# Kernel optimization log

Hardware: AMD Instinct MI355X
Metric: run time of the kernel (lower is better)

## Reference

```python
import jax, jax.numpy as jnp
import numpy as np

QMIN_A, QMAX_A = -128.0, 127.0  # int8 activation range
QMIN_W, QMAX_W = -8, 7          # int4 weight range (values generated in-range)


def per_token_dynamic_quant(x):
    # torchao asymmetric per-token int8 quant -> dequant (fake-quant round trip)
    min_val = jnp.minimum(jnp.min(x, axis=-1, keepdims=True), 0.0)
    max_val = jnp.maximum(jnp.max(x, axis=-1, keepdims=True), 0.0)
    eps = jnp.finfo(jnp.float32).eps
    scale = jnp.maximum((max_val - min_val) / (QMAX_A - QMIN_A), eps)
    dmin = min_val / scale
    dmax = max_val / scale
    zp = jnp.where((QMIN_A + dmin) + (QMAX_A + dmax) > 0.0,
                   QMIN_A - dmin, QMAX_A - dmax)
    zp = jnp.round(jnp.clip(zp, QMIN_A, QMAX_A))
    q = jnp.clip(jnp.round(x / scale) + zp, QMIN_A, QMAX_A)
    return (q - zp) * scale


def setup_inputs() -> dict:
    key = jax.random.key(0)
    k1, k2, k3 = jax.random.split(key, 3)
    B, S, IN, OUT, G = 4, 2048, 4096, 11008, 256
    input = jax.random.normal(k1, (B, S, IN), dtype=jnp.float32)
    # int4 weights stored as int8-range ints in [-8, 7]
    weight = jax.random.randint(k2, (OUT, IN), QMIN_W, QMAX_W + 1, dtype=jnp.int32)
    scales = jax.random.uniform(k3, (OUT, IN // G), dtype=jnp.float32) * 0.01 + 1e-4
    zeros = jnp.zeros((OUT, IN // G), dtype=jnp.float32)
    return {"input": input, "weight": weight, "scales": scales,
            "zeros": zeros, "groupsize": G}


def reference(input, weight, scales, zeros, groupsize):
    # per-token int8 dynamic fake-quant of activations
    x = per_token_dynamic_quant(input.astype(jnp.float32))
    # groupwise int4 dequant of weights: (w - zero) * scale per group
    O, I = weight.shape
    w = weight.reshape(O, I // groupsize, groupsize).astype(jnp.float32)
    w_dq = ((w - zeros[:, :, None]) * scales[:, :, None]).reshape(O, I)
    # linear: [B,S,I] @ [O,I]^T -> [B,S,O]
    out = jnp.einsum('bsi,oi->bso', x, w_dq)
    return out.astype(input.dtype)
```

## Files before the change

kernel.cpp:

```cpp
#include <hip/hip_runtime.h>
#include <cstdint>
#include <cstddef>

#define M_TOK 8192
#define K_IN  4096
#define N_OUT 11008
#define GRP   256
#define NGRP  (K_IN / GRP)
#define NT_K  (K_IN / 64)

typedef float f32x4   __attribute__((ext_vector_type(4)));
typedef short bf16x8  __attribute__((ext_vector_type(8)));

__device__ inline unsigned short f2bf(float f) {
    uint32_t u = __float_as_uint(f);
    uint32_t r = (u + 0x7fffu + ((u >> 16) & 1u)) >> 16;
    return (unsigned short)r;
}

__global__ __launch_bounds__(256)
void quant_kernel(const float* __restrict__ x, unsigned short* __restrict__ qx)
{
    const int t   = blockIdx.x;
    const int tid = threadIdx.x;
    const float* xr = x + (size_t)t * K_IN;

    float4 v[4];
    float mn = 0.0f, mx = 0.0f;
    #pragma unroll
    for (int j = 0; j < 4; ++j) {
        v[j] = ((const float4*)xr)[j * 256 + tid];
        mn = fminf(mn, fminf(fminf(v[j].x, v[j].y), fminf(v[j].z, v[j].w)));
        mx = fmaxf(mx, fmaxf(fmaxf(v[j].x, v[j].y), fmaxf(v[j].z, v[j].w)));
    }
    #pragma unroll
    for (int off = 32; off > 0; off >>= 1) {
        mn = fminf(mn, __shfl_xor(mn, off));
        mx = fmaxf(mx, __shfl_xor(mx, off));
    }
    __shared__ float smn[4], smx[4];
    if ((tid & 63) == 0) { smn[tid >> 6] = mn; smx[tid >> 6] = mx; }
    __syncthreads();
    mn = fminf(fminf(smn[0], smn[1]), fminf(smn[2], smn[3]));
    mx = fmaxf(fmaxf(smx[0], smx[1]), fmaxf(smx[2], smx[3]));

    const float scale = fmaxf((mx - mn) / 255.0f, 1.1920929e-7f);
    const float dmin  = mn / scale;
    const float dmax  = mx / scale;
    float zp = (((-128.0f + dmin) + (127.0f + dmax)) > 0.0f) ? (-128.0f - dmin)
                                                             : (127.0f - dmax);
    zp = rintf(fminf(fmaxf(zp, -128.0f), 127.0f));

    unsigned short* qr = qx + (size_t)t * K_IN;
    #pragma unroll
    for (int j = 0; j < 4; ++j) {
        float q0 = fminf(fmaxf(rintf(v[j].x / scale) + zp, -128.0f), 127.0f);
        float q1 = fminf(fmaxf(rintf(v[j].y / scale) + zp, -128.0f), 127.0f);
        float q2 = fminf(fmaxf(rintf(v[j].z / scale) + zp, -128.0f), 127.0f);
        float q3 = fminf(fmaxf(rintf(v[j].w / scale) + zp, -128.0f), 127.0f);
        ushort4 o;
        o.x = f2bf((q0 - zp) * scale);
        o.y = f2bf((q1 - zp) * scale);
        o.z = f2bf((q2 - zp) * scale);
        o.w = f2bf((q3 - zp) * scale);
        ((ushort4*)qr)[j * 256 + tid] = o;
    }
}

__global__ __launch_bounds__(256)
void wprep_kernel(const int* __restrict__ w, const float* __restrict__ scales,
                  const float* __restrict__ zeros, unsigned short* __restrict__ wdq)
{
    const size_t idx  = (size_t)blockIdx.x * 256 + threadIdx.x;
    const size_t base = idx * 4;
    const int o = (int)(base >> 12);
    const int k = (int)(base & 4095);
    const int g = k >> 8;
    const float s = scales[o * NGRP + g];
    const float z = zeros [o * NGRP + g];
    const int4 wi = *(const int4*)(w + base);
    ushort4 out;
    out.x = f2bf(((float)wi.x - z) * s);
    out.y = f2bf(((float)wi.y - z) * s);
    out.z = f2bf(((float)wi.z - z) * s);
    out.w = f2bf(((float)wi.w - z) * s);
    *(ushort4*)(wdq + base) = out;
}


#define PH_SYNC_IN()  do { __builtin_amdgcn_sched_barrier(0); \
                           __builtin_amdgcn_s_barrier(); \
                           asm volatile("s_waitcnt lgkmcnt(0)" ::: "memory"); \
                           __builtin_amdgcn_sched_barrier(0); } while (0)
#define PH_SYNC_OUT() do { __builtin_amdgcn_sched_barrier(0); \
                           __builtin_amdgcn_s_barrier(); } while (0)

__device__ __forceinline__ void stage_a_half(unsigned short* dst,
                                             const unsigned short* __restrict__ A,
                                             int bm, int k0, int half, int tid)
{
    #pragma unroll
    for (int i = 0; i < 2; ++i) {
        const int c  = i * 512 + tid;
        const int lr = c >> 3;
        const int cc = c & 7;
        const int gc = cc ^ (lr & 7);
        const int gr = ((lr >> 6) << 7) + (half << 6) + (lr & 63);
        __builtin_amdgcn_global_load_lds(
            (const __attribute__((address_space(1))) void*)(A + (size_t)(bm + gr) * K_IN + k0 + (gc << 3)),
            (__attribute__((address_space(3))) void*)(dst + (size_t)c * 8),
            16, 0, 0);
    }
}

__device__ __forceinline__ void stage_b_half(unsigned short* dst,
                                             const unsigned short* __restrict__ B,
                                             int bn, int k0, int half, int tid)
{
    #pragma unroll
    for (int i = 0; i < 2; ++i) {
        const int c  = i * 512 + tid;
        const int lr = c >> 3;
        const int cc = c & 7;
        const int gc = cc ^ (lr & 7);
        const int gr = ((lr >> 5) << 6) + (half << 5) + (lr & 31);
        __builtin_amdgcn_global_load_lds(
            (const __attribute__((address_space(1))) void*)(B + (size_t)(bn + gr) * K_IN + k0 + (gc << 3)),
            (__attribute__((address_space(3))) void*)(dst + (size_t)c * 8),
            16, 0, 0);
    }
}

__device__ __forceinline__ void ld_afrag(bf16x8 (&a)[4][2], const unsigned short* Ah,
                                         int wr, int lrow, int khi)
{
    #pragma unroll
    for (int mi = 0; mi < 4; ++mi) {
        const int lr = wr * 64 + mi * 16 + lrow;
        #pragma unroll
        for (int kk = 0; kk < 2; ++kk) {
            const int sc = (kk * 4 + khi) ^ (lr & 7);
            a[mi][kk] = *(const bf16x8*)(Ah + lr * 64 + sc * 8);
        }
    }
}

__device__ __forceinline__ void ld_bfrag(bf16x8 (&b)[2][2], const unsigned short* Bh,
                                         int wc, int lrow, int khi)
{
    #pragma unroll
    for (int ni = 0; ni < 2; ++ni) {
        const int lr = wc * 32 + ni * 16 + lrow;
        #pragma unroll
        for (int kk = 0; kk < 2; ++kk) {
            const int sc = (kk * 4 + khi) ^ (lr & 7);
            b[ni][kk] = *(const bf16x8*)(Bh + lr * 64 + sc * 8);
        }
    }
}

template<int MH, int NH>
__device__ __forceinline__ void mfma_quad(f32x4 (&acc)[8][4],
                                          const bf16x8 (&a)[4][2],
                                          const bf16x8 (&b)[2][2])
{
    __builtin_amdgcn_s_setprio(1);
    #pragma unroll
    for (int kk = 0; kk < 2; ++kk)
        #pragma unroll
        for (int mi = 0; mi < 4; ++mi)
            #pragma unroll
            for (int ni = 0; ni < 2; ++ni)
                acc[MH * 4 + mi][NH * 2 + ni] =
                    __builtin_amdgcn_mfma_f32_16x16x32_bf16(
                        a[mi][kk], b[ni][kk], acc[MH * 4 + mi][NH * 2 + ni], 0, 0, 0);
    __builtin_amdgcn_s_setprio(0);
}

__global__ __launch_bounds__(512, 2)
void gemm_kernel(const unsigned short* __restrict__ A,
                 const unsigned short* __restrict__ B,
                 float* __restrict__ C)
{
    __shared__ unsigned short As[2][2][128 * 64];
    __shared__ unsigned short Bs[2][2][128 * 64];

    const int tid  = threadIdx.x;
    const int lane = tid & 63;
    const int wave = tid >> 6;
    const int wr   = wave >> 2;
    const int wc   = wave & 3;
    const int lrow = lane & 15;
    const int khi  = lane >> 4;

    const int bid = blockIdx.x;
    const int swz = (bid & 7) * 172 + (bid >> 3);
    const int bm  = (swz / 43) * 256;
    const int bn  = (swz % 43) * 256;

    stage_a_half(&As[0][0][0], A, bm, 0, 0, tid);
    stage_b_half(&Bs[0][0][0], B, bn, 0, 0, tid);
    stage_a_half(&As[0][1][0], A, bm, 0, 1, tid);
    stage_b_half(&Bs[0][1][0], B, bn, 0, 1, tid);
    stage_a_half(&As[1][0][0], A, bm, 64, 0, tid);
    stage_b_half(&Bs[1][1][0], B, bn, 64, 1, tid);
    stage_a_half(&As[1][1][0], A, bm, 64, 1, tid);
    asm volatile("s_waitcnt vmcnt(6)" ::: "memory");
    __builtin_amdgcn_sched_barrier(0);
    __builtin_amdgcn_s_barrier();

    f32x4 acc[8][4] = {};
    int buf = 0;

    for (int t = 0; t < NT_K; ++t) {
        const int k1 = (t + 1) << 6;
        const int k2 = (t + 2) << 6;
        const bool p1 = t < NT_K - 1;
        const bool p2 = t < NT_K - 2;
        bf16x8 a[4][2], b[2][2];

        ld_afrag(a, &As[buf][0][0], wr, lrow, khi);
        ld_bfrag(b, &Bs[buf][0][0], wc, lrow, khi);
        if (p1) stage_b_half(&Bs[buf ^ 1][0][0], B, bn, k1, 0, tid);
        PH_SYNC_IN();
        mfma_quad<0, 0>(acc, a, b);
        PH_SYNC_OUT();

        ld_bfrag(b, &Bs[buf][1][0], wc, lrow, khi);
        if (p2) stage_a_half(&As[buf][0][0], A, bm, k2, 0, tid);
        PH_SYNC_IN();
        mfma_quad<0, 1>(acc, a, b);
        PH_SYNC_OUT();

        ld_afrag(a, &As[buf][1][0], wr, lrow, khi);
        if (p2) stage_b_half(&Bs[buf][1][0], B, bn, k2, 1, tid);
        PH_SYNC_IN();
        mfma_quad<1, 1>(acc, a, b);
        PH_SYNC_OUT();

        ld_bfrag(b, &Bs[buf][0][0], wc, lrow, khi);
        if (p2) stage_a_half(&As[buf][1][0], A, bm, k2, 1, tid);
        if (p2)      { asm volatile("s_waitcnt vmcnt(6)" ::: "memory"); }
        else if (p1) { asm volatile("s_waitcnt vmcnt(0)" ::: "memory"); }
        PH_SYNC_IN();
        mfma_quad<1, 0>(acc, a, b);
        PH_SYNC_OUT();

        buf ^= 1;
    }

    const int crow = khi * 4;
    #pragma unroll
    for (int mi = 0; mi < 8; ++mi) {
        #pragma unroll
        for (int ni = 0; ni < 4; ++ni) {
            const f32x4 v = acc[mi][ni];
            const int m0 = bm + wr * 128 + mi * 16 + crow;
            const int n0 = bn + wc * 64 + ni * 16 + lrow;
            #pragma unroll
            for (int r = 0; r < 4; ++r)
                C[(size_t)(m0 + r) * N_OUT + n0] = v[r];
        }
    }
}

extern "C" void kernel_launch(void* const* d_in, const int* in_sizes, int n_in,
                              void* d_out, int out_size, void* d_ws, size_t ws_size,
                              hipStream_t stream)
{
    const float* x      = (const float*)d_in[0];
    const int*   w      = (const int*)  d_in[1];
    const float* scales = (const float*)d_in[2];
    const float* zeros  = (const float*)d_in[3];
    float* out = (float*)d_out;

    unsigned short* qx  = (unsigned short*)d_ws;
    unsigned short* wdq = qx + (size_t)M_TOK * K_IN;

    quant_kernel<<<M_TOK, 256, 0, stream>>>(x, qx);
    wprep_kernel<<<(int)(((size_t)N_OUT * K_IN / 4) / 256), 256, 0, stream>>>(w, scales, zeros, wdq);
    gemm_kernel<<<1376, 512, 0, stream>>>(qx, wdq, out);
}
```

Baseline: 1.336 ms.

## Restructure GEMM main loop with register double-buffered fragments and fewer barriers

Rewrites the bf16 MFMA GEMM k-loop so LDS fragments for the next k-tile are loaded into a second register set while the current tile's MFMAs run. The loop is unrolled by two with a templated buffer index. The per-phase double barriers and explicit lgkmcnt waits are replaced by a single barrier per phase, and the global-to-LDS staging order and vmcnt thresholds are reshuffled. This aims to hide LDS read latency and cut synchronisation overhead. It costs more VGPRs, which may hurt occupancy at 2 blocks per CU, and it relies on the compiler's implicit lgkmcnt waits, so the correctness of the hand-tuned wait counts is fragile.

```diff
diff --git a/kernel.cpp b/kernel.cpp
--- a/kernel.cpp
+++ b/kernel.cpp
@@ -11,6 +11,9 @@
 
 typedef float f32x4   __attribute__((ext_vector_type(4)));
 typedef short bf16x8  __attribute__((ext_vector_type(8)));
+
+#define WAITV(N) asm volatile("s_waitcnt vmcnt(" #N ")" ::: "memory")
+#define BAR()    __builtin_amdgcn_s_barrier()
 
 __device__ inline unsigned short f2bf(float f) {
     uint32_t u = __float_as_uint(f);
@@ -88,13 +91,6 @@
 }
 
 
-#define PH_SYNC_IN()  do { __builtin_amdgcn_sched_barrier(0); \
-                           __builtin_amdgcn_s_barrier(); \
-                           asm volatile("s_waitcnt lgkmcnt(0)" ::: "memory"); \
-                           __builtin_amdgcn_sched_barrier(0); } while (0)
-#define PH_SYNC_OUT() do { __builtin_amdgcn_sched_barrier(0); \
-                           __builtin_amdgcn_s_barrier(); } while (0)
-
 __device__ __forceinline__ void stage_a_half(unsigned short* dst,
                                              const unsigned short* __restrict__ A,
                                              int bm, int k0, int half, int tid)
@@ -177,13 +173,61 @@
     __builtin_amdgcn_s_setprio(0);
 }
 
+template<int BUF>
+__device__ __forceinline__ void ktile_body(
+    int t, const unsigned short* __restrict__ A, const unsigned short* __restrict__ B,
+    unsigned short* Asb, unsigned short* Bsb,
+    int bm, int bn, int tid, int wr, int wc, int lrow, int khi,
+    f32x4 (&acc)[8][4],
+    bf16x8 (&a_cur)[4][2], bf16x8 (&b_cur)[2][2],
+    bf16x8 (&a_nxt)[4][2], bf16x8 (&b_nxt)[2][2])
+{
+    const bool p1 = t < NT_K - 1;
+    const bool p2 = t < NT_K - 2;
+    unsigned short* AsC = Asb + BUF * 16384;
+    unsigned short* BsC = Bsb + BUF * 16384;
+    unsigned short* AsN = Asb + (BUF ^ 1) * 16384;
+    unsigned short* BsN = Bsb + (BUF ^ 1) * 16384;
+
+    if (p1) {
+        stage_b_half(BsN,        B, bn, (t + 1) << 6, 0, tid);
+        stage_a_half(AsN + 8192, A, bm, (t + 1) << 6, 1, tid);
+        WAITV(8);
+    } else {
+        WAITV(0);
+    }
+    BAR();
+    mfma_quad<0, 0>(acc, a_cur, b_cur);
+
+    bf16x8 b1[2][2], a1[4][2];
+    ld_bfrag(b1, BsC + 8192, wc, lrow, khi);
+    ld_afrag(a1, AsC + 8192, wr, lrow, khi);
+    if (p2)      { stage_a_half(AsC, A, bm, (t + 2) << 6, 0, tid); WAITV(8); }
+    else if (p1) { WAITV(6); }
+    BAR();
+    mfma_quad<0, 1>(acc, a_cur, b1);
+
+    if (p1) ld_afrag(a_nxt, AsN, wr, lrow, khi);
+    if (p2)      { WAITV(4); }
+    else if (p1) { WAITV(2); }
+    BAR();
+    mfma_quad<1, 1>(acc, a1, b1);
+
+    if (p1) ld_bfrag(b_nxt, BsN, wc, lrow, khi);
+    if (p2) stage_b_half(BsC + 8192, B, bn, (t + 2) << 6, 1, tid);
+    BAR();
+    mfma_quad<1, 0>(acc, a1, b_cur);
+}
+
 __global__ __launch_bounds__(512, 2)
 void gemm_kernel(const unsigned short* __restrict__ A,
                  const unsigned short* __restrict__ B,
                  float* __restrict__ C)
 {
-    __shared__ unsigned short As[2][2][128 * 64];
-    __shared__ unsigned short Bs[2][2][128 * 64];
+    __shared__ unsigned short As[2][2][8192];
+    __shared__ unsigned short Bs[2][2][8192];
+    unsigned short* Asb = &As[0][0][0];
+    unsigned short* Bsb = &Bs[0][0][0];
 
     const int tid  = threadIdx.x;
     const int lane = tid & 63;
@@ -198,55 +242,25 @@
     const int bm  = (swz / 43) * 256;
     const int bn  = (swz % 43) * 256;
 
-    stage_a_half(&As[0][0][0], A, bm, 0, 0, tid);
-    stage_b_half(&Bs[0][0][0], B, bn, 0, 0, tid);
-    stage_a_half(&As[0][1][0], A, bm, 0, 1, tid);
-    stage_b_half(&Bs[0][1][0], B, bn, 0, 1, tid);
-    stage_a_half(&As[1][0][0], A, bm, 64, 0, tid);
-    stage_b_half(&Bs[1][1][0], B, bn, 64, 1, tid);
-    stage_a_half(&As[1][1][0], A, bm, 64, 1, tid);
-    asm volatile("s_waitcnt vmcnt(6)" ::: "memory");
-    __builtin_amdgcn_sched_barrier(0);
-    __builtin_amdgcn_s_barrier();
+    stage_a_half(Asb,                A, bm, 0,  0, tid);
+    stage_b_half(Bsb,                B, bn, 0,  0, tid);
+    stage_a_half(Asb + 8192,         A, bm, 0,  1, tid);
+    stage_b_half(Bsb + 8192,         B, bn, 0,  1, tid);
+    stage_a_half(Asb + 16384,        A, bm, 64, 0, tid);
+    stage_b_half(Bsb + 16384 + 8192, B, bn, 64, 1, tid);
+    WAITV(8);
+    BAR();
 
     f32x4 acc[8][4] = {};
-    int buf = 0;
-
-    for (int t = 0; t < NT_K; ++t) {
-        const int k1 = (t + 1) << 6;
-        const int k2 = (t + 2) << 6;
-        const bool p1 = t < NT_K - 1;
-        const bool p2 = t < NT_K - 2;
-        bf16x8 a[4][2], b[2][2];
-
-        ld_afrag(a, &As[buf][0][0], wr, lrow, khi);
-        ld_bfrag(b, &Bs[buf][0][0], wc, lrow, khi);
-        if (p1) stage_b_half(&Bs[buf ^ 1][0][0], B, bn, k1, 0, tid);
-        PH_SYNC_IN();
-        mfma_quad<0, 0>(acc, a, b);
-        PH_SYNC_OUT();
-
-        ld_bfrag(b, &Bs[buf][1][0], wc, lrow, khi);
-        if (p2) stage_a_half(&As[buf][0][0], A, bm, k2, 0, tid);
-        PH_SYNC_IN();
-        mfma_quad<0, 1>(acc, a, b);
-        PH_SYNC_OUT();
-
-        ld_afrag(a, &As[buf][1][0], wr, lrow, khi);
-        if (p2) stage_b_half(&Bs[buf][1][0], B, bn, k2, 1, tid);
-        PH_SYNC_IN();
-        mfma_quad<1, 1>(acc, a, b);
-        PH_SYNC_OUT();
-
-        ld_bfrag(b, &Bs[buf][0][0], wc, lrow, khi);
-        if (p2) stage_a_half(&As[buf][1][0], A, bm, k2, 1, tid);
-        if (p2)      { asm volatile("s_waitcnt vmcnt(6)" ::: "memory"); }
-        else if (p1) { asm volatile("s_waitcnt vmcnt(0)" ::: "memory"); }
-        PH_SYNC_IN();
-        mfma_quad<1, 0>(acc, a, b);
-        PH_SYNC_OUT();
-
-        buf ^= 1;
+    bf16x8 aA[4][2], bA[2][2], aB[4][2], bB[2][2];
+    ld_afrag(aA, Asb, wr, lrow, khi);
+    ld_bfrag(bA, Bsb, wc, lrow, khi);
+
+    for (int t = 0; t < NT_K; t += 2) {
+        ktile_body<0>(t,     A, B, Asb, Bsb, bm, bn, tid, wr, wc, lrow, khi,
+                      acc, aA, bA, aB, bB);
+        ktile_body<1>(t + 1, A, B, Asb, Bsb, bm, bn, tid, wr, wc, lrow, khi,
+                      acc, aB, bB, aA, bA);
     }
 
     const int crow = khi * 4;
```

Result: slower. 3.652 ms (+173.4%).
